# Kernel tuning notes

Hardware: AMD Instinct MI355X
Metric: run time of the kernel (lower is better)

Reference implementation:

```python
import jax, jax.numpy as jnp
import numpy as np
from jax import lax

B, L, V, E, H = 256, 512, 256, 256, 1024


def setup_inputs() -> dict:
    key = jax.random.key(0)
    k1, k2, k3, k4, k5 = jax.random.split(key, 5)
    x = jax.random.randint(k1, (B, L), 0, V, dtype=jnp.int64)
    hidden = jnp.zeros((B, H), dtype=jnp.float32)
    emb_table = jax.random.normal(k2, (V, E), dtype=jnp.float32)  # nn.Embedding default init ~N(0,1)
    W_e = 0.01 * jax.random.normal(k3, (E, H), dtype=jnp.float32)
    W_h = 0.01 * jax.random.normal(k4, (H, H), dtype=jnp.float32)
    W_o = 0.01 * jax.random.normal(k5, (H, V), dtype=jnp.float32)
    return {"x": x, "hidden": hidden, "emb_table": emb_table, "W_e": W_e, "W_h": W_h, "W_o": W_o}


def reference(x, hidden, emb_table, W_e, W_h, W_o):
    # Precompute input projection for all timesteps in one batched GEMM:
    # emb_table[x] : [B, L, E];  x_proj : [L, B, H] (time-major for scan)
    x_proj = jnp.einsum('ble,eh->lbh', emb_table[x], W_e)

    def step(h_prev, x_t):
        h_t = jnp.tanh(x_t + h_prev @ W_h)  # [B, H]
        return h_t, h_t

    final_hidden, outs = lax.scan(step, hidden, x_proj)  # outs: [L, B, H]
    # logits: [B, L, V]
    logits = jnp.einsum('lbh,hv->blv', outs, W_o)
    return logits, final_hidden
```

## Files before the change

kernel.cpp:

```cpp
#include <hip/hip_runtime.h>
#include <hip/hip_bf16.h>
#include <math.h>

#define B_ 256
#define L_ 512
#define V_ 256
#define E_ 256
#define H_ 1024

typedef float  f32x4  __attribute__((ext_vector_type(4)));
typedef short  bf16x8 __attribute__((ext_vector_type(8)));

static __device__ __forceinline__ ushort f2bf(float v) {
    __hip_bfloat16 b = __float2bfloat16(v);
    return *reinterpret_cast<ushort*>(&b);
}

static __device__ __forceinline__ void load_lds16(const void* g, void* l) {
    __builtin_amdgcn_global_load_lds(
        (const __attribute__((address_space(1))) void*)(g),
        (__attribute__((address_space(3))) void*)(l), 16, 0, 0);
}

__global__ void k_transpose_bf16(const float* __restrict__ in, ushort* __restrict__ out,
                                 int R, int C) {
    __shared__ float tile[64][65];
    int bx = blockIdx.x;
    int by = blockIdx.y;
    int tid = threadIdx.x;
    int g = tid >> 6, l = tid & 63;
    for (int i = 0; i < 16; ++i) {
        int r = g * 16 + i;
        tile[r][l] = in[(size_t)(by * 64 + r) * C + bx * 64 + l];
    }
    __syncthreads();
    for (int i = 0; i < 16; ++i) {
        int c = g * 16 + i;
        out[(size_t)(bx * 64 + c) * R + by * 64 + l] = f2bf(tile[l][c]);
    }
}

__global__ void k_f32_to_bf16(const float* __restrict__ in, ushort* __restrict__ out, int n) {
    int i = blockIdx.x * blockDim.x + threadIdx.x;
    if (i < n) out[i] = f2bf(in[i]);
}

__global__ void k_zero(unsigned* __restrict__ p, int n) {
    int i = blockIdx.x * blockDim.x + threadIdx.x;
    if (i < n) p[i] = 0u;
}

__global__ void k_proj(const float* __restrict__ emb, const float* __restrict__ We,
                       float* __restrict__ proj) {
    __shared__ float er[E_];
    int t = blockIdx.x;
    int h = blockIdx.y * 256 + threadIdx.x;
    er[threadIdx.x] = emb[t * E_ + threadIdx.x];
    __syncthreads();
    float acc = 0.f;
#pragma unroll 8
    for (int e = 0; e < E_; ++e) acc += er[e] * We[(size_t)e * H_ + h];
    proj[(size_t)t * H_ + h] = acc;
}

__global__ __launch_bounds__(256, 1) void k_scan(
    const int* __restrict__ x, const float* __restrict__ proj,
    const ushort* __restrict__ WhT, const ushort* __restrict__ WoT,
    ushort* __restrict__ ring, float* __restrict__ logits,
    float* __restrict__ final_h, unsigned* __restrict__ flags)
{
    __shared__ ushort lds_w[32 * 1024];
    __shared__ ushort lds_h[32 * 1024];
    __shared__ float  red[4 * 64 * 4];
    __shared__ ushort stile[32 * 32];

    int tid = threadIdx.x;
    int w = tid >> 6, lane = tid & 63;
    int l15 = lane & 15, l4 = lane >> 4;
    int bid = blockIdx.x;
    int rg = bid & 7;
    int cg = bid >> 3;
    int r0 = rg * 32, c0 = cg * 32;

    {
        const char* wsrc = (const char*)(WhT + (size_t)c0 * H_);
        char* wd = (char*)lds_w;
        for (int i = 0; i < 16; ++i) {
            int chunk = (w * 16 + i) * 1024;
            int o = chunk + lane * 16;
            int row = o >> 11, b = o & 2047;
            int so = row * 2048 + (b ^ ((row & 7) << 4));
            load_lds16(wsrc + so, wd + chunk);
        }
    }

    int a = w >> 1, bc = w & 1;
    int arow = a * 16 + l15;
    int brow = bc * 16 + l15;
    const char* ha = (const char*)lds_h + arow * 2048;
    const char* wa = (const char*)lds_w + brow * 2048;
    int as = (arow & 7) << 4, bs = (brow & 7) << 4;
    int gcol = c0 + bc * 16 + l15;

    int lrg = cg & 1, vcol0 = (cg >> 1) * 16;
    int srow = lrg * 16 + l15;
    const char* hbp = (const char*)lds_h + srow * 2048;
    int hs2 = (srow & 7) << 4;
    const ushort* wo = WoT + (size_t)(vcol0 + l15) * H_;

    for (int s = 0; s <= L_; ++s) {
        if (s > 0) {
            if (tid == 0) {
                const unsigned* fp = &flags[rg * 512 + (s - 1)];
                unsigned v;
                do {
                    asm volatile("global_load_dword %0, %1, off sc0 sc1\n\t"
                                 "s_waitcnt vmcnt(0)"
                                 : "=v"(v) : "v"(fp) : "memory");
                    if (v >= 32u) break;
                    __builtin_amdgcn_s_sleep(1);
                } while (1);
            }
        }
        __syncthreads();

        {
            const char* hsrc = (const char*)(ring + (size_t)(s & 1) * B_ * H_
                                             + (size_t)r0 * H_) + tid * 16;
            f32x4 tv[16];
#pragma unroll
            for (int i = 0; i < 16; ++i) {
                asm volatile("global_load_dwordx4 %0, %1, off sc0 sc1"
                             : "=v"(tv[i]) : "v"(hsrc + i * 4096) : "memory");
            }
            asm volatile("s_waitcnt vmcnt(0)" ::: "memory");
#pragma unroll
            for (int i = 0; i < 16; ++i) {
                int o = i * 4096 + tid * 16;
                int row = o >> 11, b = o & 2047;
                *(f32x4*)((char*)lds_h + row * 2048 + (b ^ ((row & 7) << 4))) = tv[i];
            }
        }
        __syncthreads();

        if (s < L_) {
            float pv[4];
#pragma unroll
            for (int j = 0; j < 4; ++j) {
                int grow = r0 + a * 16 + l4 * 4 + j;
                pv[j] = proj[(size_t)x[grow * L_ + s] * H_ + gcol];
            }
            f32x4 acc = {0.f, 0.f, 0.f, 0.f};
#pragma unroll
            for (int kk = 0; kk < 32; ++kk) {
                int kb = (kk * 32 + l4 * 8) * 2;
                bf16x8 af = *(const bf16x8*)(ha + (kb ^ as));
                bf16x8 bf = *(const bf16x8*)(wa + (kb ^ bs));
                acc = __builtin_amdgcn_mfma_f32_16x16x32_bf16(af, bf, acc, 0, 0, 0);
            }
#pragma unroll
            for (int j = 0; j < 4; ++j) {
                int lrow = a * 16 + l4 * 4 + j;
                float hv = tanhf(acc[j] + pv[j]);
                stile[lrow * 32 + bc * 16 + l15] = f2bf(hv);
                if (s == L_ - 1) final_h[(size_t)(r0 + lrow) * H_ + gcol] = hv;
            }
            __syncthreads();
            if (tid < 128) {
                int row = tid >> 2, seg = tid & 3;
                f32x4 d = *(const f32x4*)&stile[row * 32 + seg * 8];
                char* dst = (char*)(ring + (size_t)((s + 1) & 1) * B_ * H_
                                    + (size_t)(r0 + row) * H_ + c0 + seg * 8);
                asm volatile("global_store_dwordx4 %0, %1, off sc0 sc1"
                             :: "v"(dst), "v"(d) : "memory");
            }
            asm volatile("s_waitcnt vmcnt(0)" ::: "memory");
            __syncthreads();
            if (tid == 0) atomicAdd(&flags[rg * 512 + s], 1u);
        }

        if (s > 0) {
            f32x4 lacc = {0.f, 0.f, 0.f, 0.f};
#pragma unroll
            for (int kk = 0; kk < 8; ++kk) {
                int k = w * 256 + kk * 32 + l4 * 8;
                bf16x8 af = *(const bf16x8*)(hbp + ((2 * k) ^ hs2));
                bf16x8 bf = *(const bf16x8*)(wo + k);
                lacc = __builtin_amdgcn_mfma_f32_16x16x32_bf16(af, bf, lacc, 0, 0, 0);
            }
#pragma unroll
            for (int j = 0; j < 4; ++j) red[(w * 64 + lane) * 4 + j] = lacc[j];
            __syncthreads();
            if (w == 0) {
                int growb = r0 + lrg * 16 + l4 * 4;
#pragma unroll
                for (int j = 0; j < 4; ++j) {
                    float ssum = red[(0 * 64 + lane) * 4 + j] + red[(1 * 64 + lane) * 4 + j]
                               + red[(2 * 64 + lane) * 4 + j] + red[(3 * 64 + lane) * 4 + j];
                    logits[((size_t)(growb + j) * L_ + (s - 1)) * V_ + vcol0 + l15] = ssum;
                }
            }
        }
    }
}

extern "C" void kernel_launch(void* const* d_in, const int* in_sizes, int n_in,
                              void* d_out, int out_size, void* d_ws, size_t ws_size,
                              hipStream_t stream)
{
    const int*   x   = (const int*)d_in[0];
    const float* hid = (const float*)d_in[1];
    const float* emb = (const float*)d_in[2];
    const float* We  = (const float*)d_in[3];
    const float* Wh  = (const float*)d_in[4];
    const float* Wo  = (const float*)d_in[5];

    float* logits  = (float*)d_out;
    float* final_h = logits + (size_t)B_ * L_ * V_;

    char* ws = (char*)d_ws;
    float*    proj  = (float*)(ws);
    ushort*   WhT   = (ushort*)(ws + (1u << 20));
    ushort*   WoT   = (ushort*)(ws + 3u * (1u << 20));
    ushort*   ring  = (ushort*)(ws + 3u * (1u << 20) + (1u << 19));
    unsigned* flags = (unsigned*)(ws + 4u * (1u << 20) + (1u << 19));

    k_zero<<<dim3(16), 256, 0, stream>>>(flags, 8 * 512);
    k_transpose_bf16<<<dim3(16, 16), 256, 0, stream>>>(Wh, WhT, H_, H_);
    k_transpose_bf16<<<dim3(4, 16),  256, 0, stream>>>(Wo, WoT, H_, V_);
    k_f32_to_bf16<<<dim3(1024), 256, 0, stream>>>(hid, ring, B_ * H_);
    k_proj<<<dim3(256, 4), 256, 0, stream>>>(emb, We, proj);

    k_scan<<<dim3(256), 256, 0, stream>>>(x, proj, WhT, WoT, ring,
                                          logits, final_h, flags);
}
```

Measured before the change: 2.237 ms.

## Overlap logits projection with barrier wait, use per-block flag slots

Restructures the persistent scan loop so that the output-logits MFMA for the previous step runs on waves 1-3 while wave 0 polls for the next hidden state. Each row group now has one flag word per column block, written with a plain store and checked with a wave-wide ballot, replacing the atomic counter and sleep-based spin. The proj gather is hoisted ahead of the wait, and the recurrent GEMM is split across two accumulators to shorten the MFMA dependency chain. In exchange there is a larger flag array, one extra loop iteration, and a logits store that lags by two steps.

```diff
diff --git a/kernel.cpp b/kernel.cpp
--- a/kernel.cpp
+++ b/kernel.cpp
@@ -7,6 +7,7 @@
 #define V_ 256
 #define E_ 256
 #define H_ 1024
+#define NSTEP_ 513
 
 typedef float  f32x4  __attribute__((ext_vector_type(4)));
 typedef short  bf16x8 __attribute__((ext_vector_type(8)));
@@ -14,12 +15,6 @@
 static __device__ __forceinline__ ushort f2bf(float v) {
     __hip_bfloat16 b = __float2bfloat16(v);
     return *reinterpret_cast<ushort*>(&b);
-}
-
-static __device__ __forceinline__ void load_lds16(const void* g, void* l) {
-    __builtin_amdgcn_global_load_lds(
-        (const __attribute__((address_space(1))) void*)(g),
-        (__attribute__((address_space(3))) void*)(l), 16, 0, 0);
 }
 
 __global__ void k_transpose_bf16(const float* __restrict__ in, ushort* __restrict__ out,
@@ -71,7 +66,7 @@
 {
     __shared__ ushort lds_w[32 * 1024];
     __shared__ ushort lds_h[32 * 1024];
-    __shared__ float  red[4 * 64 * 4];
+    __shared__ float  red[256 * 5];
     __shared__ ushort stile[32 * 32];
 
     int tid = threadIdx.x;
@@ -90,7 +85,9 @@
             int o = chunk + lane * 16;
             int row = o >> 11, b = o & 2047;
             int so = row * 2048 + (b ^ ((row & 7) << 4));
-            load_lds16(wsrc + so, wd + chunk);
+            __builtin_amdgcn_global_load_lds(
+                (const __attribute__((address_space(1))) void*)(wsrc + so),
+                (__attribute__((address_space(3))) void*)(wd + chunk), 16, 0, 0);
         }
     }
 
@@ -107,32 +104,65 @@
     const char* hbp = (const char*)lds_h + srow * 2048;
     int hs2 = (srow & 7) << 4;
     const ushort* wo = WoT + (size_t)(vcol0 + l15) * H_;
-
-    for (int s = 0; s <= L_; ++s) {
-        if (s > 0) {
-            if (tid == 0) {
-                const unsigned* fp = &flags[rg * 512 + (s - 1)];
-                unsigned v;
-                do {
-                    asm volatile("global_load_dword %0, %1, off sc0 sc1\n\t"
-                                 "s_waitcnt vmcnt(0)"
-                                 : "=v"(v) : "v"(fp) : "memory");
-                    if (v >= 32u) break;
-                    __builtin_amdgcn_s_sleep(1);
-                } while (1);
-            }
+    int bbase = (w == 1) ? 0 : (w == 2) ? 11 : 22;
+    int bcnt  = (w == 3) ? 10 : 11;
+
+    for (int s = 0; s <= NSTEP_; ++s) {
+        float pv[4];
+        if (s < L_) {
+#pragma unroll
+            for (int j = 0; j < 4; ++j) {
+                int grow = r0 + a * 16 + l4 * 4 + j;
+                pv[j] = proj[(size_t)x[grow * L_ + s] * H_ + gcol];
+            }
+        }
+
+        if (w == 0) {
+            if (s >= 1 && s <= L_) {
+                const unsigned* fp = flags + ((size_t)rg * NSTEP_ + s) * 32 + lane;
+                unsigned v = 1u;
+                while (true) {
+                    if (lane < 32) {
+                        asm volatile("global_load_dword %0, %1, off sc0 sc1\n\t"
+                                     "s_waitcnt vmcnt(0)"
+                                     : "=v"(v) : "v"(fp) : "memory");
+                    }
+                    if (__ballot(v != 0u) == ~0ull) break;
+                }
+            }
+        } else if (s >= 2) {
+            f32x4 lacc = {0.f, 0.f, 0.f, 0.f};
+            for (int kk = 0; kk < bcnt; ++kk) {
+                int k = (bbase + kk) * 32 + l4 * 8;
+                bf16x8 af = *(const bf16x8*)(hbp + ((2 * k) ^ hs2));
+                bf16x8 bf = *(const bf16x8*)(wo + k);
+                lacc = __builtin_amdgcn_mfma_f32_16x16x32_bf16(af, bf, lacc, 0, 0, 0);
+            }
+#pragma unroll
+            for (int j = 0; j < 4; ++j) red[tid * 5 + j] = lacc[j];
         }
         __syncthreads();
 
-        {
+        f32x4 tv[16];
+        if (s <= L_) {
             const char* hsrc = (const char*)(ring + (size_t)(s & 1) * B_ * H_
                                              + (size_t)r0 * H_) + tid * 16;
-            f32x4 tv[16];
 #pragma unroll
             for (int i = 0; i < 16; ++i) {
                 asm volatile("global_load_dwordx4 %0, %1, off sc0 sc1"
                              : "=v"(tv[i]) : "v"(hsrc + i * 4096) : "memory");
             }
+        }
+        if (w == 0 && s >= 2) {
+            int growb = r0 + lrg * 16 + l4 * 4;
+#pragma unroll
+            for (int j = 0; j < 4; ++j) {
+                float ssum = red[(64 + lane) * 5 + j] + red[(128 + lane) * 5 + j]
+                           + red[(192 + lane) * 5 + j];
+                logits[((size_t)(growb + j) * L_ + (s - 2)) * V_ + vcol0 + l15] = ssum;
+            }
+        }
+        if (s <= L_) {
             asm volatile("s_waitcnt vmcnt(0)" ::: "memory");
 #pragma unroll
             for (int i = 0; i < 16; ++i) {
@@ -144,24 +174,23 @@
         __syncthreads();
 
         if (s < L_) {
-            float pv[4];
-#pragma unroll
-            for (int j = 0; j < 4; ++j) {
-                int grow = r0 + a * 16 + l4 * 4 + j;
-                pv[j] = proj[(size_t)x[grow * L_ + s] * H_ + gcol];
-            }
-            f32x4 acc = {0.f, 0.f, 0.f, 0.f};
-#pragma unroll
-            for (int kk = 0; kk < 32; ++kk) {
-                int kb = (kk * 32 + l4 * 8) * 2;
-                bf16x8 af = *(const bf16x8*)(ha + (kb ^ as));
-                bf16x8 bf = *(const bf16x8*)(wa + (kb ^ bs));
-                acc = __builtin_amdgcn_mfma_f32_16x16x32_bf16(af, bf, acc, 0, 0, 0);
+            f32x4 acc0 = {0.f, 0.f, 0.f, 0.f};
+            f32x4 acc1 = {0.f, 0.f, 0.f, 0.f};
+#pragma unroll
+            for (int kk = 0; kk < 32; kk += 2) {
+                int kb0 = (kk * 32 + l4 * 8) * 2;
+                int kb1 = ((kk + 1) * 32 + l4 * 8) * 2;
+                bf16x8 af0 = *(const bf16x8*)(ha + (kb0 ^ as));
+                bf16x8 bf0 = *(const bf16x8*)(wa + (kb0 ^ bs));
+                bf16x8 af1 = *(const bf16x8*)(ha + (kb1 ^ as));
+                bf16x8 bf1 = *(const bf16x8*)(wa + (kb1 ^ bs));
+                acc0 = __builtin_amdgcn_mfma_f32_16x16x32_bf16(af0, bf0, acc0, 0, 0, 0);
+                acc1 = __builtin_amdgcn_mfma_f32_16x16x32_bf16(af1, bf1, acc1, 0, 0, 0);
             }
 #pragma unroll
             for (int j = 0; j < 4; ++j) {
                 int lrow = a * 16 + l4 * 4 + j;
-                float hv = tanhf(acc[j] + pv[j]);
+                float hv = tanhf((acc0[j] + acc1[j]) + pv[j]);
                 stile[lrow * 32 + bc * 16 + l15] = f2bf(hv);
                 if (s == L_ - 1) final_h[(size_t)(r0 + lrow) * H_ + gcol] = hv;
             }
@@ -176,29 +205,11 @@
             }
             asm volatile("s_waitcnt vmcnt(0)" ::: "memory");
             __syncthreads();
-            if (tid == 0) atomicAdd(&flags[rg * 512 + s], 1u);
-        }
-
-        if (s > 0) {
-            f32x4 lacc = {0.f, 0.f, 0.f, 0.f};
-#pragma unroll
-            for (int kk = 0; kk < 8; ++kk) {
-                int k = w * 256 + kk * 32 + l4 * 8;
-                bf16x8 af = *(const bf16x8*)(hbp + ((2 * k) ^ hs2));
-                bf16x8 bf = *(const bf16x8*)(wo + k);
-                lacc = __builtin_amdgcn_mfma_f32_16x16x32_bf16(af, bf, lacc, 0, 0, 0);
-            }
-#pragma unroll
-            for (int j = 0; j < 4; ++j) red[(w * 64 + lane) * 4 + j] = lacc[j];
-            __syncthreads();
-            if (w == 0) {
-                int growb = r0 + lrg * 16 + l4 * 4;
-#pragma unroll
-                for (int j = 0; j < 4; ++j) {
-                    float ssum = red[(0 * 64 + lane) * 4 + j] + red[(1 * 64 + lane) * 4 + j]
-                               + red[(2 * 64 + lane) * 4 + j] + red[(3 * 64 + lane) * 4 + j];
-                    logits[((size_t)(growb + j) * L_ + (s - 1)) * V_ + vcol0 + l15] = ssum;
-                }
+            if (tid == 0) {
+                unsigned* fdst = flags + ((size_t)rg * NSTEP_ + (s + 1)) * 32 + cg;
+                unsigned one = 1u;
+                asm volatile("global_store_dword %0, %1, off sc0 sc1"
+                             :: "v"(fdst), "v"(one) : "memory");
             }
         }
     }
@@ -225,7 +236,7 @@
     ushort*   ring  = (ushort*)(ws + 3u * (1u << 20) + (1u << 19));
     unsigned* flags = (unsigned*)(ws + 4u * (1u << 20) + (1u << 19));
 
-    k_zero<<<dim3(16), 256, 0, stream>>>(flags, 8 * 512);
+    k_zero<<<dim3(NSTEP_), 256, 0, stream>>>(flags, 8 * NSTEP_ * 32);
     k_transpose_bf16<<<dim3(16, 16), 256, 0, stream>>>(Wh, WhT, H_, H_);
     k_transpose_bf16<<<dim3(4, 16),  256, 0, stream>>>(Wo, WoT, H_, V_);
     k_f32_to_bf16<<<dim3(1024), 256, 0, stream>>>(hid, ring, B_ * H_);
```

Result: slower. 2.433 ms (+8.8%).
